# Optimization experiments

Hardware: AMD Instinct MI355X
Metric: run time of the kernel (lower is better)

Reference implementation:

```python
import jax, jax.numpy as jnp
import numpy as np

N = 100000       # num nodes
E = 1600000      # num edges
D_IN = 32
D_HID = 32
D_OUT = 32
K = 3            # Chebyshev order (number of terms)


def setup_inputs() -> dict:
    key = jax.random.key(0)
    k1, k2, k3, k4, k5, k6 = jax.random.split(key, 6)
    x = jax.random.normal(k1, (N, D_IN), dtype=jnp.float32)
    edge_index = jax.random.randint(k2, (2, E), 0, N, dtype=jnp.int64)
    s1 = 1.0 / np.sqrt(D_IN)
    s2 = 1.0 / np.sqrt(D_HID)
    W1 = jax.random.uniform(k3, (K, D_IN, D_HID), jnp.float32, -s1, s1)
    b1 = jax.random.uniform(k4, (D_HID,), jnp.float32, -s1, s1)
    W2 = jax.random.uniform(k5, (K, D_HID, D_OUT), jnp.float32, -s2, s2)
    b2 = jax.random.uniform(k6, (D_OUT,), jnp.float32, -s2, s2)
    return {"x": x, "edge_index": edge_index, "W1": W1, "b1": b1, "W2": W2, "b2": b2}


def _prop(x, row, col, w):
    # L_hat @ x : gather along col, scale by edge weight, scatter-add to row.
    # (diagonal of the rescaled Laplacian cancels to 0 in PyG ChebConv with
    #  sym normalization and lambda_max=2, so only off-diagonal edges remain)
    return jax.ops.segment_sum(w[:, None] * x[col], row, num_segments=N)


def _cheb_conv(x, row, col, w, W, b):
    # Chebyshev recurrence: Tx0 = x, Tx1 = L_hat x, Tx_k = 2 L_hat Tx_{k-1} - Tx_{k-2}
    k_terms = W.shape[0]
    Tx0 = x
    out = Tx0 @ W[0]
    if k_terms > 1:
        Tx1 = _prop(Tx0, row, col, w)
        out = out + Tx1 @ W[1]
        for k in range(2, k_terms):
            Tx2 = 2.0 * _prop(Tx1, row, col, w) - Tx0
            out = out + Tx2 @ W[k]
            Tx0, Tx1 = Tx1, Tx2
    return out + b


def reference(x, edge_index, W1, b1, W2, b2):
    row, col = edge_index[0], edge_index[1]
    mask = (row != col).astype(x.dtype)            # remove_self_loops
    deg = jax.ops.segment_sum(mask, row, num_segments=N)
    dinv = jnp.where(deg > 0, 1.0 / jnp.sqrt(jnp.maximum(deg, 1.0)), 0.0)
    w = -mask * dinv[row] * dinv[col]              # scaled Laplacian off-diagonal weights
    x0 = x
    h = jax.nn.relu(_cheb_conv(x, row, col, w, W1, b1))
    h = _cheb_conv(h, row, col, w, W2, b2)
    return h + x0
```

## Files before the change

kernel.cpp:

```cpp
#include <hip/hip_runtime.h>

#define NN 100000
#define EE 1600000
#define DD 32
#define NBUK 391
#define BROWS 256
#define TILE 4096
#define NT 391
#define BCAP2 4864

#define TOTP   106176
#define ENT2SZ 2084352

__constant__ int c_cap[9]   = {0, 2944, 56320, 43520, 2944, 256, 64, 64, 64};
__constant__ int c_pbase[9] = {0, 0, 2944, 59264, 102784, 105728, 105984, 106048, 106112};
__constant__ int c_ebase[9] = {0, 0, 23552, 924672, 1969152, 2063360, 2073600, 2076672, 2080256};

typedef unsigned int uint;
typedef unsigned short ushort;
typedef unsigned char uchar;
typedef __attribute__((ext_vector_type(8))) short bf16x8;
typedef __attribute__((ext_vector_type(4))) float f32x4;
typedef __attribute__((ext_vector_type(2))) float f32x2;

typedef __attribute__((ext_vector_type(4))) uint u32x4v;
typedef __attribute__((ext_vector_type(2))) uint u32x2v;
typedef __attribute__((ext_vector_type(2))) int i32x2v;
typedef __attribute__((ext_vector_type(4))) float f32x4v;

__device__ __forceinline__ uint4 ntld(const uint4* p) {
    u32x4v v = __builtin_nontemporal_load((const u32x4v*)p);
    uint4 r; r.x = v.x; r.y = v.y; r.z = v.z; r.w = v.w; return r;
}
__device__ __forceinline__ uint2 ntld(const uint2* p) {
    u32x2v v = __builtin_nontemporal_load((const u32x2v*)p);
    uint2 r; r.x = v.x; r.y = v.y; return r;
}
__device__ __forceinline__ int2 ntld(const int2* p) {
    i32x2v v = __builtin_nontemporal_load((const i32x2v*)p);
    int2 r; r.x = v.x; r.y = v.y; return r;
}
__device__ __forceinline__ float4 ntld(const float4* p) {
    f32x4v v = __builtin_nontemporal_load((const f32x4v*)p);
    float4 r; r.x = v.x; r.y = v.y; r.z = v.z; r.w = v.w; return r;
}
__device__ __forceinline__ int   ntld(const int* p)   { return __builtin_nontemporal_load(p); }
__device__ __forceinline__ float ntld(const float* p) { return __builtin_nontemporal_load(p); }
__device__ __forceinline__ void ntst(uint4* p, uint4 v) {
    u32x4v w; w.x = v.x; w.y = v.y; w.z = v.z; w.w = v.w;
    __builtin_nontemporal_store(w, (u32x4v*)p);
}
__device__ __forceinline__ void ntst(int4* p, int4 v) {
    uint4 u; u.x = (uint)v.x; u.y = (uint)v.y; u.z = (uint)v.z; u.w = (uint)v.w;
    ntst((uint4*)p, u);
}
__device__ __forceinline__ void ntst(uint2* p, uint2 v) {
    u32x2v w; w.x = v.x; w.y = v.y;
    __builtin_nontemporal_store(w, (u32x2v*)p);
}
__device__ __forceinline__ void ntst(int* p, int v)     { __builtin_nontemporal_store(v, p); }
__device__ __forceinline__ void ntst(float* p, float v) { __builtin_nontemporal_store(v, p); }

__device__ __forceinline__ ushort f2b(float f) {
    uint u = __float_as_uint(f);
    u += 0x7fffu + ((u >> 16) & 1u);
    return (ushort)(u >> 16);
}
__device__ __forceinline__ uint f2e4(float f) {
    uint u = __float_as_uint(f);
    uint s = (u >> 24) & 0x80u;
    float a = fabsf(f) * 0x1p-120f;
    uint g = __float_as_uint(a);
    g += 0x7FFFFu + ((g >> 20) & 1u);
    uint m = g >> 20;
    if (m > 0x7Eu) m = 0x7Eu;
    return s | m;
}
__device__ __forceinline__ bf16x8 as_bf16x8(uint4 v) {
    union { uint4 u; bf16x8 b; } cv; cv.u = v; return cv.b;
}
__device__ __forceinline__ void acc8(float* acc, uint2 v) {
#pragma unroll
    for (int wi = 0; wi < 2; ++wi) {
        uint w = (&v.x)[wi];
        f32x2 lo = __builtin_amdgcn_cvt_pk_f32_fp8((int)w, false);
        f32x2 hi = __builtin_amdgcn_cvt_pk_f32_fp8((int)w, true);
        acc[wi * 4 + 0] += lo.x;
        acc[wi * 4 + 1] += lo.y;
        acc[wi * 4 + 2] += hi.x;
        acc[wi * 4 + 3] += hi.y;
    }
}


__global__ void k_part(const int* __restrict__ ei, int* __restrict__ gtail,
                       int* __restrict__ pairs) {
    __shared__ int hist[512];
    __shared__ int gbase[512];
    int t = threadIdx.x;
    hist[t] = 0; hist[t + 256] = 0;
    __syncthreads();
    int e0 = blockIdx.x * TILE;
    int pk[16], rk[16], bb[16];
#pragma unroll
    for (int k = 0; k < 16; ++k) {
        int e = e0 + t + k * 256;
        bb[k] = -1;
        if (e < EE) {
            int r = ntld(ei + e), c = ntld(ei + EE + e);
            if (r != c) {
                bb[k] = r >> 8;
                pk[k] = (r & (BROWS - 1)) | (c << 8);
                rk[k] = atomicAdd(&hist[bb[k]], 1);
            }
        }
    }
    __syncthreads();
    for (int q = t; q < NBUK; q += 256) {
        int cnt = hist[q];
        gbase[q] = cnt ? atomicAdd(&gtail[q * 16], cnt) : 0;
    }
    __syncthreads();
#pragma unroll
    for (int k = 0; k < 16; ++k) {
        if (bb[k] >= 0) {
            int pos = gbase[bb[k]] + rk[k];
            if (pos < BCAP2) pairs[bb[k] * BCAP2 + pos] = pk[k];
        }
    }
}


__global__ void k_build2(const int* __restrict__ gtail, const int* __restrict__ pairs,
                         float* __restrict__ dinv, int* __restrict__ ctail,
                         int* __restrict__ ent2, int2* __restrict__ pdesc) {
    __shared__ int lcnt[BROWS];
    __shared__ int lh[16];
    __shared__ int gb[16];
    __shared__ int sofs[BROWS];
    __shared__ uchar scls[BROWS];
    __shared__ int slab[BROWS * 64];
    int b = blockIdx.x, t = threadIdx.x;
    lcnt[t] = 0;
    if (t < 16) lh[t] = 0;
    for (int i = t; i < BROWS * 64; i += 256) slab[i] = NN;
    __syncthreads();
    int cnt = gtail[b * 16]; if (cnt > BCAP2) cnt = BCAP2;
    const int* pp = pairs + b * BCAP2;
    for (int i = t; i < cnt; i += 256) {
        int v = ntld(pp + i);
        int lr = v & (BROWS - 1);
        int pos = atomicAdd(&lcnt[lr], 1);
        if (pos < 64) slab[(lr << 6) + pos] = (int)((uint)v >> 8);
    }
    __syncthreads();
    int n = b * BROWS + t;
    int cpl = 0, lrank = 0;
    if (n < NN) {
        int d = lcnt[t];
        int ms = d > 64 ? 64 : d;
        int cls = (ms + 7) >> 3;
        cpl = cls ? cls : 1;
        dinv[n] = d > 0 ? rsqrtf((float)d) : 0.0f;
        lrank = atomicAdd(&lh[cpl], 1);
    }
    __syncthreads();
    if (t < 16) gb[t] = lh[t] ? atomicAdd(&ctail[t], lh[t]) : 0;
    __syncthreads();
    int myofs = -1;
    if (n < NN) {
        int rank = gb[cpl] + lrank;
        if (rank < c_cap[cpl]) {
            myofs = c_ebase[cpl] + rank * (cpl << 3);
            int2 pv; pv.x = n; pv.y = (myofs >> 3) | (cpl << 24);
            pdesc[c_pbase[cpl] + rank] = pv;
        }
    }
    sofs[t] = myofs;
    scls[t] = (uchar)cpl;
    __syncthreads();
    for (int i = t; i < BROWS * 16; i += 256) {
        int row = i >> 4, piece = i & 15;
        int ofs = sofs[row];
        if (ofs >= 0 && piece < (scls[row] << 1)) {
            int4 v = *(const int4*)&slab[(row << 6) + (piece << 2)];
            ntst((int4*)&ent2[ofs + (piece << 2)], v);
        }
    }
}


__global__ void k_cvt(const float* __restrict__ x, uint2* __restrict__ xb,
                      uint* __restrict__ xb8, const float* __restrict__ dinv,
                      const float* __restrict__ W1, const float* __restrict__ W2,
                      ushort* __restrict__ wb1, ushort* __restrict__ wb2,
                      uint* __restrict__ t1b8, uint* __restrict__ hb8) {
    if (blockIdx.x == (NN * DD / 4) / 256) {
        for (int i = threadIdx.x; i < 6144; i += 256) {
            const float* W = W1; ushort* wb = wb1;
            int ii = i;
            if (ii >= 3072) { ii -= 3072; W = W2; wb = wb2; }
            int term = ii >> 10, rem = ii & 1023;
            int h = rem >> 9, lane = (rem >> 3) & 63, j = rem & 7;
            int k = ((lane >> 4) << 3) + j;
            int col = (h << 4) | (lane & 15);
            float val = W[term * 1024 + k * 32 + col];
            if (term == 0) val -= W[2 * 1024 + k * 32 + col];
            wb[ii] = f2b(val);
        }
        return;
    }
    if (blockIdx.x == 0) {
        if (threadIdx.x >= 64 && threadIdx.x < 72) xb8[NN * 8 + threadIdx.x - 64] = 0;
        if (threadIdx.x >= 72 && threadIdx.x < 80) t1b8[NN * 8 + threadIdx.x - 72] = 0;
        if (threadIdx.x >= 80 && threadIdx.x < 88) hb8[NN * 8 + threadIdx.x - 80] = 0;
    }
    int tid = blockIdx.x * blockDim.x + threadIdx.x;
    if (tid >= NN * DD / 4) return;
    float4 v = ntld(((const float4*)x) + tid);
    uint2 b;
    b.x = (uint)f2b(v.x) | ((uint)f2b(v.y) << 16);
    b.y = (uint)f2b(v.z) | ((uint)f2b(v.w) << 16);
    ntst(xb + tid, b);
    float dv = dinv[tid >> 3];
    xb8[tid] = f2e4(dv * v.x) | (f2e4(dv * v.y) << 8)
             | (f2e4(dv * v.z) << 16) | (f2e4(dv * v.w) << 24);
}


__global__ void k_prop(const int2* __restrict__ pdesc, const int* __restrict__ ent2,
                       const float* __restrict__ dinv,
                       const uint2* __restrict__ src8d,
                       uint2* __restrict__ dst8d,
                       uint4* __restrict__ dstbq,
                       float alpha) {
    int tid = blockIdx.x * blockDim.x + threadIdx.x;
    int g = tid >> 3;
    int sub = tid & 3, h = (tid >> 2) & 1;
    int2 pd = ntld(pdesc + g);
    int cls = (pd.y >> 24) & 15;
    if (cls == 0) return;
    int n = pd.x;
    const int* ep = ent2 + ((size_t)(pd.y & 0xFFFFFF) << 3);
    int mr = cls << 3;
    float acc[8] = {0, 0, 0, 0, 0, 0, 0, 0};
    for (int i = h * 8; i < mr; i += 16) {
        uint4 C0 = ntld((const uint4*)(ep + i));
        uint4 C1 = ntld((const uint4*)(ep + i + 4));
        uint2 v0 = src8d[(C0.x << 2) + sub];
        uint2 v1 = src8d[(C0.y << 2) + sub];
        uint2 v2 = src8d[(C0.z << 2) + sub];
        uint2 v3 = src8d[(C0.w << 2) + sub];
        uint2 v4 = src8d[(C1.x << 2) + sub];
        uint2 v5 = src8d[(C1.y << 2) + sub];
        uint2 v6 = src8d[(C1.z << 2) + sub];
        uint2 v7 = src8d[(C1.w << 2) + sub];
        acc8(acc, v0); acc8(acc, v1); acc8(acc, v2); acc8(acc, v3);
        acc8(acc, v4); acc8(acc, v5); acc8(acc, v6); acc8(acc, v7);
    }
    float dn = dinv[n];
    float s = -alpha * dn;
#pragma unroll
    for (int k = 0; k < 8; ++k)
        acc[k] = s * (acc[k] + __shfl_xor(acc[k], 4, 64));
    if (h == 0) {
        uint4 ob;
#pragma unroll
        for (int wi = 0; wi < 4; ++wi)
            (&ob.x)[wi] = (uint)f2b(acc[wi * 2]) | ((uint)f2b(acc[wi * 2 + 1]) << 16);
        ntst(dstbq + (n << 2) + sub, ob);
    } else if (dst8d) {
        uint2 o8;
        o8.x = f2e4(dn * acc[0]) | (f2e4(dn * acc[1]) << 8)
             | (f2e4(dn * acc[2]) << 16) | (f2e4(dn * acc[3]) << 24);
        o8.y = f2e4(dn * acc[4]) | (f2e4(dn * acc[5]) << 8)
             | (f2e4(dn * acc[6]) << 16) | (f2e4(dn * acc[7]) << 24);
        ntst(dst8d + (n << 2) + sub, o8);
    }
}


__global__ void k_comb(const uint4* __restrict__ t0, const uint4* __restrict__ t1,
                       const uint4* __restrict__ t2, const ushort* __restrict__ wb,
                       const float* __restrict__ bias, const float* __restrict__ residf,
                       const float* __restrict__ dinv,
                       float* __restrict__ outf, ushort* __restrict__ outb,
                       uchar* __restrict__ outb8, int do_relu) {
    int lane = threadIdx.x & 63;
    int wid = threadIdx.x >> 6;
    int n0 = (blockIdx.x * 4 + wid) << 6;
    if (n0 >= NN) return;
    int q = lane >> 4, lr = lane & 15;
    const uint4* wq = (const uint4*)wb;
    bf16x8 bf[3][2];
#pragma unroll
    for (int t = 0; t < 3; ++t)
#pragma unroll
        for (int h = 0; h < 2; ++h)
            bf[t][h] = as_bf16x8(wq[((t * 2 + h) << 6) + lane]);
    float bias0 = bias[lr], bias1 = bias[16 + lr];
    uint4 z; z.x = 0; z.y = 0; z.z = 0; z.w = 0;
#pragma unroll
    for (int mt = 0; mt < 4; ++mt) {
        int nb = n0 + (mt << 4);
        int row = nb + lr;
        bool ok = row < NN;
        int ai = (row << 2) + q;
        bf16x8 a0 = as_bf16x8(ok ? ntld(t0 + ai) : z);
        bf16x8 a1 = as_bf16x8(ok ? ntld(t1 + ai) : z);
        bf16x8 a2 = as_bf16x8(ok ? ntld(t2 + ai) : z);
        f32x4 c0 = {0.f, 0.f, 0.f, 0.f};
        f32x4 c1 = {0.f, 0.f, 0.f, 0.f};
        c0 = __builtin_amdgcn_mfma_f32_16x16x32_bf16(a0, bf[0][0], c0, 0, 0, 0);
        c0 = __builtin_amdgcn_mfma_f32_16x16x32_bf16(a1, bf[1][0], c0, 0, 0, 0);
        c0 = __builtin_amdgcn_mfma_f32_16x16x32_bf16(a2, bf[2][0], c0, 0, 0, 0);
        c1 = __builtin_amdgcn_mfma_f32_16x16x32_bf16(a0, bf[0][1], c1, 0, 0, 0);
        c1 = __builtin_amdgcn_mfma_f32_16x16x32_bf16(a1, bf[1][1], c1, 0, 0, 0);
        c1 = __builtin_amdgcn_mfma_f32_16x16x32_bf16(a2, bf[2][1], c1, 0, 0, 0);
#pragma unroll
        for (int r = 0; r < 4; ++r) {
            int node = nb + (q << 2) + r;
            if (node >= NN) continue;
            float v0 = c0[r] + bias0;
            float v1 = c1[r] + bias1;
            if (do_relu) { v0 = fmaxf(v0, 0.0f); v1 = fmaxf(v1, 0.0f); }
            if (outb) {
                float dv = dinv[node];
                outb[node * DD + lr] = f2b(v0);
                outb[node * DD + 16 + lr] = f2b(v1);
                outb8[node * DD + lr] = (uchar)f2e4(dv * v0);
                outb8[node * DD + 16 + lr] = (uchar)f2e4(dv * v1);
            } else {
                ntst(outf + node * DD + lr, v0 + ntld(residf + node * DD + lr));
                ntst(outf + node * DD + 16 + lr, v1 + ntld(residf + node * DD + 16 + lr));
            }
        }
    }
}


extern "C" void kernel_launch(void* const* d_in, const int* in_sizes, int n_in,
                              void* d_out, int out_size, void* d_ws, size_t ws_size,
                              hipStream_t stream) {
    const float* x  = (const float*)d_in[0];
    const int*   ei = (const int*)d_in[1];
    const float* W1 = (const float*)d_in[2];
    const float* b1 = (const float*)d_in[3];
    const float* W2 = (const float*)d_in[4];
    const float* b2 = (const float*)d_in[5];
    float* out = (float*)d_out;

    char* wsp = (char*)d_ws;
    size_t off = 0;
    auto take = [&](size_t bytes) {
        char* p = wsp + off;
        off = (off + bytes + 255) & ~(size_t)255;
        return p;
    };
    int*    ctrl  = (int*)take((size_t)(NBUK * 16 + 16) * 4);
    int*    gtail = ctrl;
    int*    ctail = ctrl + NBUK * 16;
    int2*   pdesc = (int2*)take((size_t)TOTP * 8);
    float*  dinv  = (float*)take((size_t)NN * 4);
    ushort* wb1   = (ushort*)take((size_t)3072 * 2);
    ushort* wb2   = (ushort*)take((size_t)3072 * 2);
    int*    pairs = (int*)take((size_t)NBUK * BCAP2 * 4);
    int*    ent2  = (int*)take((size_t)ENT2SZ * 4);
    ushort* xb    = (ushort*)take((size_t)NN * DD * 2);
    ushort* t1b   = (ushort*)take((size_t)NN * DD * 2);
    ushort* t2b   = (ushort*)take((size_t)NN * DD * 2);
    ushort* hb    = (ushort*)take((size_t)NN * DD * 2);
    uchar*  xb8   = (uchar*)take((size_t)(NN + 1) * DD);
    uchar*  t1b8  = (uchar*)take((size_t)(NN + 1) * DD);
    uchar*  hb8   = (uchar*)take((size_t)(NN + 1) * DD);

    size_t msz = (size_t)((char*)pdesc - (char*)ctrl) + (size_t)TOTP * 8;
    hipMemsetAsync(ctrl, 0, msz, stream);

    k_part  <<<NT, 256, 0, stream>>>(ei, gtail, pairs);
    k_build2<<<NBUK, 256, 0, stream>>>(gtail, pairs, dinv, ctail, ent2, pdesc);
    k_cvt   <<<NN * DD / 4 / 256 + 1, 256, 0, stream>>>(x, (uint2*)xb, (uint*)xb8, dinv,
                                                        W1, W2, wb1, wb2,
                                                        (uint*)t1b8, (uint*)hb8);

    const int pgrid = TOTP * 8 / 256;
    const int mgrid = (NN + 255) / 256;
    k_prop<<<pgrid, 256, 0, stream>>>(pdesc, ent2, dinv, (const uint2*)xb8,
                                      (uint2*)t1b8, (uint4*)t1b, 1.0f);
    k_prop<<<pgrid, 256, 0, stream>>>(pdesc, ent2, dinv, (const uint2*)t1b8,
                                      nullptr, (uint4*)t2b, 2.0f);
    k_comb<<<mgrid, 256, 0, stream>>>((const uint4*)xb, (const uint4*)t1b,
                                      (const uint4*)t2b, wb1, b1, nullptr, dinv,
                                      nullptr, hb, hb8, 1);
    k_prop<<<pgrid, 256, 0, stream>>>(pdesc, ent2, dinv, (const uint2*)hb8,
                                      (uint2*)t1b8, (uint4*)t1b, 1.0f);
    k_prop<<<pgrid, 256, 0, stream>>>(pdesc, ent2, dinv, (const uint2*)t1b8,
                                      nullptr, (uint4*)t2b, 2.0f);
    k_comb<<<mgrid, 256, 0, stream>>>((const uint4*)hb, (const uint4*)t1b,
                                      (const uint4*)t2b, wb2, b2, x, dinv,
                                      out, nullptr, nullptr, 0);
}
```

Before: 230.1 us.

## Fuse propagation and combine kernels into one cooperative persistent kernel

Replaces the four propagation launches and two combine launches with a single cooperative kernel. It uses grid-stride loops for each phase and grid.sync barriers between phases. The aim is to remove per-launch overhead and the tail idle time between dependent kernels. In exchange, grid-wide barriers can cost more than a launch boundary. The grid is capped at occupancy times 256 blocks, which may lower parallelism and per-thread latency hiding in the gather-heavy propagation phases.

```diff
diff --git a/kernel.cpp b/kernel.cpp
--- a/kernel.cpp
+++ b/kernel.cpp
@@ -1,4 +1,7 @@
 #include <hip/hip_runtime.h>
+#include <hip/hip_cooperative_groups.h>
+
+namespace cg = cooperative_groups;
 
 #define NN 100000
 #define EE 1600000
@@ -228,68 +231,66 @@
 }
 
 
-__global__ void k_prop(const int2* __restrict__ pdesc, const int* __restrict__ ent2,
-                       const float* __restrict__ dinv,
-                       const uint2* __restrict__ src8d,
-                       uint2* __restrict__ dst8d,
-                       uint4* __restrict__ dstbq,
-                       float alpha) {
-    int tid = blockIdx.x * blockDim.x + threadIdx.x;
-    int g = tid >> 3;
-    int sub = tid & 3, h = (tid >> 2) & 1;
-    int2 pd = ntld(pdesc + g);
-    int cls = (pd.y >> 24) & 15;
-    if (cls == 0) return;
-    int n = pd.x;
-    const int* ep = ent2 + ((size_t)(pd.y & 0xFFFFFF) << 3);
-    int mr = cls << 3;
-    float acc[8] = {0, 0, 0, 0, 0, 0, 0, 0};
-    for (int i = h * 8; i < mr; i += 16) {
-        uint4 C0 = ntld((const uint4*)(ep + i));
-        uint4 C1 = ntld((const uint4*)(ep + i + 4));
-        uint2 v0 = src8d[(C0.x << 2) + sub];
-        uint2 v1 = src8d[(C0.y << 2) + sub];
-        uint2 v2 = src8d[(C0.z << 2) + sub];
-        uint2 v3 = src8d[(C0.w << 2) + sub];
-        uint2 v4 = src8d[(C1.x << 2) + sub];
-        uint2 v5 = src8d[(C1.y << 2) + sub];
-        uint2 v6 = src8d[(C1.z << 2) + sub];
-        uint2 v7 = src8d[(C1.w << 2) + sub];
-        acc8(acc, v0); acc8(acc, v1); acc8(acc, v2); acc8(acc, v3);
-        acc8(acc, v4); acc8(acc, v5); acc8(acc, v6); acc8(acc, v7);
-    }
-    float dn = dinv[n];
-    float s = -alpha * dn;
-#pragma unroll
-    for (int k = 0; k < 8; ++k)
-        acc[k] = s * (acc[k] + __shfl_xor(acc[k], 4, 64));
-    if (h == 0) {
-        uint4 ob;
-#pragma unroll
-        for (int wi = 0; wi < 4; ++wi)
-            (&ob.x)[wi] = (uint)f2b(acc[wi * 2]) | ((uint)f2b(acc[wi * 2 + 1]) << 16);
-        ntst(dstbq + (n << 2) + sub, ob);
-    } else if (dst8d) {
-        uint2 o8;
-        o8.x = f2e4(dn * acc[0]) | (f2e4(dn * acc[1]) << 8)
-             | (f2e4(dn * acc[2]) << 16) | (f2e4(dn * acc[3]) << 24);
-        o8.y = f2e4(dn * acc[4]) | (f2e4(dn * acc[5]) << 8)
-             | (f2e4(dn * acc[6]) << 16) | (f2e4(dn * acc[7]) << 24);
-        ntst(dst8d + (n << 2) + sub, o8);
-    }
-}
-
-
-__global__ void k_comb(const uint4* __restrict__ t0, const uint4* __restrict__ t1,
-                       const uint4* __restrict__ t2, const ushort* __restrict__ wb,
-                       const float* __restrict__ bias, const float* __restrict__ residf,
-                       const float* __restrict__ dinv,
-                       float* __restrict__ outf, ushort* __restrict__ outb,
-                       uchar* __restrict__ outb8, int do_relu) {
+__device__ void prop_phase(const int2* __restrict__ pdesc, const int* __restrict__ ent2,
+                           const float* __restrict__ dinv,
+                           const uint2* __restrict__ src8d,
+                           uint2* __restrict__ dst8d, uint4* __restrict__ dstbq,
+                           float alpha, int gsz) {
+    for (int u = blockIdx.x * 256 + threadIdx.x; u < TOTP * 8; u += gsz) {
+        int g = u >> 3;
+        int sub = u & 3, h = (u >> 2) & 1;
+        int2 pd = ntld(pdesc + g);
+        int cls = (pd.y >> 24) & 15;
+        if (cls == 0) continue;
+        int n = pd.x;
+        const int* ep = ent2 + ((size_t)(pd.y & 0xFFFFFF) << 3);
+        int mr = cls << 3;
+        float acc[8] = {0, 0, 0, 0, 0, 0, 0, 0};
+        for (int i = h * 8; i < mr; i += 16) {
+            uint4 C0 = ntld((const uint4*)(ep + i));
+            uint4 C1 = ntld((const uint4*)(ep + i + 4));
+            uint2 v0 = src8d[(C0.x << 2) + sub];
+            uint2 v1 = src8d[(C0.y << 2) + sub];
+            uint2 v2 = src8d[(C0.z << 2) + sub];
+            uint2 v3 = src8d[(C0.w << 2) + sub];
+            uint2 v4 = src8d[(C1.x << 2) + sub];
+            uint2 v5 = src8d[(C1.y << 2) + sub];
+            uint2 v6 = src8d[(C1.z << 2) + sub];
+            uint2 v7 = src8d[(C1.w << 2) + sub];
+            acc8(acc, v0); acc8(acc, v1); acc8(acc, v2); acc8(acc, v3);
+            acc8(acc, v4); acc8(acc, v5); acc8(acc, v6); acc8(acc, v7);
+        }
+        float dn = dinv[n];
+        float s = -alpha * dn;
+#pragma unroll
+        for (int k = 0; k < 8; ++k)
+            acc[k] = s * (acc[k] + __shfl_xor(acc[k], 4, 64));
+        if (h == 0) {
+            uint4 ob;
+#pragma unroll
+            for (int wi = 0; wi < 4; ++wi)
+                (&ob.x)[wi] = (uint)f2b(acc[wi * 2]) | ((uint)f2b(acc[wi * 2 + 1]) << 16);
+            ntst(dstbq + (n << 2) + sub, ob);
+        } else if (dst8d) {
+            uint2 o8;
+            o8.x = f2e4(dn * acc[0]) | (f2e4(dn * acc[1]) << 8)
+                 | (f2e4(dn * acc[2]) << 16) | (f2e4(dn * acc[3]) << 24);
+            o8.y = f2e4(dn * acc[4]) | (f2e4(dn * acc[5]) << 8)
+                 | (f2e4(dn * acc[6]) << 16) | (f2e4(dn * acc[7]) << 24);
+            ntst(dst8d + (n << 2) + sub, o8);
+        }
+    }
+}
+
+
+__device__ void comb_phase(const uint4* __restrict__ t0, const uint4* __restrict__ t1,
+                           const uint4* __restrict__ t2, const ushort* __restrict__ wb,
+                           const float* __restrict__ bias, const float* __restrict__ residf,
+                           const float* __restrict__ dinv,
+                           float* __restrict__ outf, ushort* __restrict__ outb,
+                           uchar* __restrict__ outb8, int do_relu, int nblk) {
     int lane = threadIdx.x & 63;
     int wid = threadIdx.x >> 6;
-    int n0 = (blockIdx.x * 4 + wid) << 6;
-    if (n0 >= NN) return;
     int q = lane >> 4, lr = lane & 15;
     const uint4* wq = (const uint4*)wb;
     bf16x8 bf[3][2];
@@ -300,42 +301,72 @@
             bf[t][h] = as_bf16x8(wq[((t * 2 + h) << 6) + lane]);
     float bias0 = bias[lr], bias1 = bias[16 + lr];
     uint4 z; z.x = 0; z.y = 0; z.z = 0; z.w = 0;
-#pragma unroll
-    for (int mt = 0; mt < 4; ++mt) {
-        int nb = n0 + (mt << 4);
-        int row = nb + lr;
-        bool ok = row < NN;
-        int ai = (row << 2) + q;
-        bf16x8 a0 = as_bf16x8(ok ? ntld(t0 + ai) : z);
-        bf16x8 a1 = as_bf16x8(ok ? ntld(t1 + ai) : z);
-        bf16x8 a2 = as_bf16x8(ok ? ntld(t2 + ai) : z);
-        f32x4 c0 = {0.f, 0.f, 0.f, 0.f};
-        f32x4 c1 = {0.f, 0.f, 0.f, 0.f};
-        c0 = __builtin_amdgcn_mfma_f32_16x16x32_bf16(a0, bf[0][0], c0, 0, 0, 0);
-        c0 = __builtin_amdgcn_mfma_f32_16x16x32_bf16(a1, bf[1][0], c0, 0, 0, 0);
-        c0 = __builtin_amdgcn_mfma_f32_16x16x32_bf16(a2, bf[2][0], c0, 0, 0, 0);
-        c1 = __builtin_amdgcn_mfma_f32_16x16x32_bf16(a0, bf[0][1], c1, 0, 0, 0);
-        c1 = __builtin_amdgcn_mfma_f32_16x16x32_bf16(a1, bf[1][1], c1, 0, 0, 0);
-        c1 = __builtin_amdgcn_mfma_f32_16x16x32_bf16(a2, bf[2][1], c1, 0, 0, 0);
-#pragma unroll
-        for (int r = 0; r < 4; ++r) {
-            int node = nb + (q << 2) + r;
-            if (node >= NN) continue;
-            float v0 = c0[r] + bias0;
-            float v1 = c1[r] + bias1;
-            if (do_relu) { v0 = fmaxf(v0, 0.0f); v1 = fmaxf(v1, 0.0f); }
-            if (outb) {
-                float dv = dinv[node];
-                outb[node * DD + lr] = f2b(v0);
-                outb[node * DD + 16 + lr] = f2b(v1);
-                outb8[node * DD + lr] = (uchar)f2e4(dv * v0);
-                outb8[node * DD + 16 + lr] = (uchar)f2e4(dv * v1);
-            } else {
-                ntst(outf + node * DD + lr, v0 + ntld(residf + node * DD + lr));
-                ntst(outf + node * DD + 16 + lr, v1 + ntld(residf + node * DD + 16 + lr));
+    for (int n0 = (blockIdx.x * 4 + wid) << 6; n0 < NN; n0 += nblk * 4 * 64) {
+#pragma unroll
+        for (int mt = 0; mt < 4; ++mt) {
+            int nb = n0 + (mt << 4);
+            int row = nb + lr;
+            bool ok = row < NN;
+            int ai = (row << 2) + q;
+            bf16x8 a0 = as_bf16x8(ok ? ntld(t0 + ai) : z);
+            bf16x8 a1 = as_bf16x8(ok ? ntld(t1 + ai) : z);
+            bf16x8 a2 = as_bf16x8(ok ? ntld(t2 + ai) : z);
+            f32x4 c0 = {0.f, 0.f, 0.f, 0.f};
+            f32x4 c1 = {0.f, 0.f, 0.f, 0.f};
+            c0 = __builtin_amdgcn_mfma_f32_16x16x32_bf16(a0, bf[0][0], c0, 0, 0, 0);
+            c0 = __builtin_amdgcn_mfma_f32_16x16x32_bf16(a1, bf[1][0], c0, 0, 0, 0);
+            c0 = __builtin_amdgcn_mfma_f32_16x16x32_bf16(a2, bf[2][0], c0, 0, 0, 0);
+            c1 = __builtin_amdgcn_mfma_f32_16x16x32_bf16(a0, bf[0][1], c1, 0, 0, 0);
+            c1 = __builtin_amdgcn_mfma_f32_16x16x32_bf16(a1, bf[1][1], c1, 0, 0, 0);
+            c1 = __builtin_amdgcn_mfma_f32_16x16x32_bf16(a2, bf[2][1], c1, 0, 0, 0);
+#pragma unroll
+            for (int r = 0; r < 4; ++r) {
+                int node = nb + (q << 2) + r;
+                if (node >= NN) continue;
+                float v0 = c0[r] + bias0;
+                float v1 = c1[r] + bias1;
+                if (do_relu) { v0 = fmaxf(v0, 0.0f); v1 = fmaxf(v1, 0.0f); }
+                if (outb) {
+                    float dv = dinv[node];
+                    outb[node * DD + lr] = f2b(v0);
+                    outb[node * DD + 16 + lr] = f2b(v1);
+                    outb8[node * DD + lr] = (uchar)f2e4(dv * v0);
+                    outb8[node * DD + 16 + lr] = (uchar)f2e4(dv * v1);
+                } else {
+                    ntst(outf + node * DD + lr, v0 + ntld(residf + node * DD + lr));
+                    ntst(outf + node * DD + 16 + lr, v1 + ntld(residf + node * DD + 16 + lr));
+                }
             }
         }
     }
+}
+
+
+__global__ void k_mega(const int2* __restrict__ pdesc, const int* __restrict__ ent2,
+                       const float* __restrict__ dinv,
+                       const uint2* __restrict__ xb8, uint2* __restrict__ t1b8,
+                       uint4* __restrict__ t1b, uint4* __restrict__ t2b,
+                       const uint4* __restrict__ xb, uint4* __restrict__ hb,
+                       uchar* __restrict__ hb8,
+                       const ushort* __restrict__ wb1, const ushort* __restrict__ wb2,
+                       const float* __restrict__ b1, const float* __restrict__ b2,
+                       const float* __restrict__ xresid, float* __restrict__ out) {
+    cg::grid_group grid = cg::this_grid();
+    int nblk = (int)gridDim.x;
+    int gsz = nblk * 256;
+    prop_phase(pdesc, ent2, dinv, xb8, t1b8, t1b, 1.0f, gsz);
+    __threadfence(); grid.sync();
+    prop_phase(pdesc, ent2, dinv, (const uint2*)t1b8, nullptr, t2b, 2.0f, gsz);
+    __threadfence(); grid.sync();
+    comb_phase(xb, (const uint4*)t1b, (const uint4*)t2b, wb1, b1, nullptr, dinv,
+               nullptr, (ushort*)hb, hb8, 1, nblk);
+    __threadfence(); grid.sync();
+    prop_phase(pdesc, ent2, dinv, (const uint2*)hb8, t1b8, t1b, 1.0f, gsz);
+    __threadfence(); grid.sync();
+    prop_phase(pdesc, ent2, dinv, (const uint2*)t1b8, nullptr, t2b, 2.0f, gsz);
+    __threadfence(); grid.sync();
+    comb_phase((const uint4*)hb, (const uint4*)t1b, (const uint4*)t2b, wb2, b2,
+               xresid, dinv, out, nullptr, nullptr, 0, nblk);
 }
 
 
@@ -383,20 +414,34 @@
                                                         W1, W2, wb1, wb2,
                                                         (uint*)t1b8, (uint*)hb8);
 
-    const int pgrid = TOTP * 8 / 256;
-    const int mgrid = (NN + 255) / 256;
-    k_prop<<<pgrid, 256, 0, stream>>>(pdesc, ent2, dinv, (const uint2*)xb8,
-                                      (uint2*)t1b8, (uint4*)t1b, 1.0f);
-    k_prop<<<pgrid, 256, 0, stream>>>(pdesc, ent2, dinv, (const uint2*)t1b8,
-                                      nullptr, (uint4*)t2b, 2.0f);
-    k_comb<<<mgrid, 256, 0, stream>>>((const uint4*)xb, (const uint4*)t1b,
-                                      (const uint4*)t2b, wb1, b1, nullptr, dinv,
-                                      nullptr, hb, hb8, 1);
-    k_prop<<<pgrid, 256, 0, stream>>>(pdesc, ent2, dinv, (const uint2*)hb8,
-                                      (uint2*)t1b8, (uint4*)t1b, 1.0f);
-    k_prop<<<pgrid, 256, 0, stream>>>(pdesc, ent2, dinv, (const uint2*)t1b8,
-                                      nullptr, (uint4*)t2b, 2.0f);
-    k_comb<<<mgrid, 256, 0, stream>>>((const uint4*)hb, (const uint4*)t1b,
-                                      (const uint4*)t2b, wb2, b2, x, dinv,
-                                      out, nullptr, nullptr, 0);
-}
+    static int maxb = -1;
+    if (maxb < 0) {
+        int mb = 0;
+        if (hipOccupancyMaxActiveBlocksPerMultiprocessor(
+                &mb, reinterpret_cast<const void*>(&k_mega), 256, 0) != hipSuccess || mb <= 0)
+            mb = 4;
+        maxb = mb;
+    }
+    int grid = maxb * 256;
+    const int full = (TOTP * 8) / 256;
+    if (grid > full) grid = full;
+
+    const int2*   a_pdesc = pdesc;  const int* a_ent2 = ent2;  const float* a_dinv = dinv;
+    const uint2*  a_xb8 = (const uint2*)xb8;
+    uint2*  a_t1b8 = (uint2*)t1b8;
+    uint4*  a_t1b  = (uint4*)t1b;   uint4* a_t2b = (uint4*)t2b;
+    const uint4* a_xb = (const uint4*)xb;
+    uint4*  a_hb = (uint4*)hb;      uchar* a_hb8 = hb8;
+    const ushort* a_wb1 = wb1;      const ushort* a_wb2 = wb2;
+    const float* a_b1 = b1;         const float* a_b2 = b2;
+    const float* a_x = x;           float* a_out = out;
+    void* kargs[] = {
+        (void*)&a_pdesc, (void*)&a_ent2, (void*)&a_dinv,
+        (void*)&a_xb8, (void*)&a_t1b8, (void*)&a_t1b, (void*)&a_t2b,
+        (void*)&a_xb, (void*)&a_hb, (void*)&a_hb8,
+        (void*)&a_wb1, (void*)&a_wb2, (void*)&a_b1, (void*)&a_b2,
+        (void*)&a_x, (void*)&a_out
+    };
+    hipLaunchCooperativeKernel(reinterpret_cast<const void*>(&k_mega),
+                               dim3(grid), dim3(256), kargs, 0, stream);
+}
```

Result: slower. 833.5 us (+262.3%).
